# Performance work log

Measured on AMD Instinct MI355X. Metric: run time of the kernel, lower is better.

Reference implementation:

```python
import jax, jax.numpy as jnp
import numpy as np

N = 8192      # nodes
F = 256       # input feature dim
D_OUT = 256   # output_dim


def setup_inputs() -> dict:
    key = jax.random.key(0)
    k1, k2, k3 = jax.random.split(key, 3)
    data = jax.random.normal(k1, (1, N, F), dtype=jnp.float32)
    # dense (normalized) adjacency; the original converts dense->sparse then matmuls,
    # which is mathematically a dense adj @ data product.
    adj = jax.random.uniform(k2, (1, N, N), dtype=jnp.float32)
    kernel = jax.random.normal(k3, (F, D_OUT), dtype=jnp.float32)
    return {"data": data, "adj": adj, "kernel": kernel}


def reference(data, adj, kernel):
    # af = adj @ data  : [N, N] @ [N, F] -> [N, F]  (neighbor aggregation)
    af = jnp.matmul(adj[0], data[0])
    # dense projection: [N, F] @ [F, D_OUT] -> [N, D_OUT]
    out = jnp.matmul(af, kernel)
    # expand batch dim back and apply activation (relu)
    return jax.nn.relu(out[None, :, :])
```

## Files before the change

kernel.cpp:

```cpp
#include <hip/hip_runtime.h>
#include <stdint.h>

#define AS1 __attribute__((address_space(1)))
#define AS3 __attribute__((address_space(3)))

typedef float f32x4 __attribute__((ext_vector_type(4)));
typedef __bf16 bf16x8 __attribute__((ext_vector_type(8)));
typedef uint32_t u32x2 __attribute__((ext_vector_type(2)));
typedef unsigned short u16;
typedef u16 u16x8 __attribute__((ext_vector_type(8)));

__device__ __forceinline__ unsigned short f2bf(float f) {
    uint32_t x = __float_as_uint(f);
    x += 0x7FFFu + ((x >> 16) & 1u);
    return (unsigned short)(x >> 16);
}
__device__ __forceinline__ float bf2f(unsigned short u) {
    return __uint_as_float((uint32_t)u << 16);
}

__device__ __forceinline__ void gload_lds16(const void* g, void* l) {
    __builtin_amdgcn_global_load_lds((const AS1 void*)g, (AS3 void*)l, 16, 0, 0);
}

__global__ __launch_bounds__(256) void wt_kernel(const float* __restrict__ W,
                                                 unsigned short* __restrict__ WT) {
    __shared__ float tile[32][33];
    const int bf = blockIdx.x & 7;
    const int bn = blockIdx.x >> 3;
    const int t = threadIdx.x;
    const int c = t & 31, r = t >> 5;
#pragma unroll
    for (int i = 0; i < 4; ++i)
        tile[r + i * 8][c] = W[(bf * 32 + r + i * 8) * 256 + bn * 32 + c];
    __syncthreads();
#pragma unroll
    for (int i = 0; i < 4; ++i)
        WT[(bn * 32 + r + i * 8) * 256 + bf * 32 + c] = f2bf(tile[c][r + i * 8]);
}

template <int LDA, int LDB, int KSTEPS>
__global__ __launch_bounds__(256) void gemm1_kernel(const float* __restrict__ A,
                                                    const unsigned short* __restrict__ B,
                                                    unsigned short* __restrict__ dkT) {
    __shared__ unsigned short Alds[32 * 64];
    __shared__ unsigned short Blds[256 * 64];

    const int t = threadIdx.x;
    const int w = t >> 6;
    const int l = t & 63;
    const int m0 = blockIdx.x * 32;

    const int ar = t >> 3;
    const int kq = t & 7;
    const float* gA = A + (size_t)(m0 + ar) * LDA + kq * 4;
    char* aw0 = (char*)Alds + ((ar * 128 + kq * 8) ^ ((ar & 7) << 4));
    char* aw1 = (char*)Alds + ((ar * 128 + 64 + kq * 8) ^ ((ar & 7) << 4));

    const int nr_base = w * 64 + (l >> 3);
    const int c16 = l & 7;

    f32x4 acc[2][4];
#pragma unroll
    for (int i = 0; i < 2; ++i)
#pragma unroll
        for (int j = 0; j < 4; ++j) acc[i][j] = (f32x4){0.f, 0.f, 0.f, 0.f};

    for (int step = 0; step < KSTEPS; ++step) {
        const int k0 = step * 64;
        __syncthreads();
#pragma unroll
        for (int i = 0; i < 8; ++i) {
            const int nr = nr_base + i * 8;
            const unsigned short* src =
                B + (size_t)nr * LDB + k0 + ((c16 ^ (nr & 7)) << 3);
            gload_lds16(src, (char*)Blds + (w * 512 + i * 64) * 16);
        }
        const f32x4 v0 = *(const f32x4*)(gA + k0);
        const f32x4 v1 = *(const f32x4*)(gA + k0 + 32);
        uint32_t p0 = (uint32_t)f2bf(v0.x) | ((uint32_t)f2bf(v0.y) << 16);
        uint32_t p1 = (uint32_t)f2bf(v0.z) | ((uint32_t)f2bf(v0.w) << 16);
        uint32_t p2 = (uint32_t)f2bf(v1.x) | ((uint32_t)f2bf(v1.y) << 16);
        uint32_t p3 = (uint32_t)f2bf(v1.z) | ((uint32_t)f2bf(v1.w) << 16);
        ((uint32_t*)aw0)[0] = p0;
        ((uint32_t*)aw0)[1] = p1;
        ((uint32_t*)aw1)[0] = p2;
        ((uint32_t*)aw1)[1] = p3;
        __syncthreads();
#pragma unroll
        for (int kh = 0; kh < 2; ++kh) {
            const int koffb = kh * 64 + ((l >> 4) << 4);
            bf16x8 af[2], bv[4];
#pragma unroll
            for (int im = 0; im < 2; ++im) {
                const int r = im * 16 + (l & 15);
                af[im] = *(const bf16x8*)((const char*)Alds +
                                          ((r * 128 + koffb) ^ ((r & 7) << 4)));
            }
#pragma unroll
            for (int jn = 0; jn < 4; ++jn) {
                const int n = w * 64 + jn * 16 + (l & 15);
                bv[jn] = *(const bf16x8*)((const char*)Blds +
                                          ((n * 128 + koffb) ^ ((n & 7) << 4)));
            }
#pragma unroll
            for (int im = 0; im < 2; ++im)
#pragma unroll
                for (int jn = 0; jn < 4; ++jn)
                    acc[im][jn] = __builtin_amdgcn_mfma_f32_16x16x32_bf16(
                        af[im], bv[jn], acc[im][jn], 0, 0, 0);
        }
    }

    __syncthreads();
    u16* T = (u16*)Blds;
#pragma unroll
    for (int im = 0; im < 2; ++im) {
        const int mq = im * 16 + ((l >> 4) << 2);
#pragma unroll
        for (int jn = 0; jn < 4; ++jn) {
            const int n = w * 64 + jn * 16 + (l & 15);
            u32x2 pk;
            pk[0] = (uint32_t)f2bf(acc[im][jn][0]) |
                    ((uint32_t)f2bf(acc[im][jn][1]) << 16);
            pk[1] = (uint32_t)f2bf(acc[im][jn][2]) |
                    ((uint32_t)f2bf(acc[im][jn][3]) << 16);
            *(u32x2*)((char*)T + n * 80 + mq * 2) = pk;
        }
    }
    __syncthreads();
    {
        const int n = t;
        const char* src = (const char*)T + n * 80;
        char* dst = (char*)(dkT + (size_t)n * 8192 + m0);
#pragma unroll
        for (int i = 0; i < 4; ++i)
            *(f32x4*)(dst + i * 16) = *(const f32x4*)(src + i * 16);
    }
}

template <int KSPLIT>
__global__ __launch_bounds__(512) void gemm2_kernel(const float* __restrict__ A,
                                                    const unsigned short* __restrict__ B,
                                                    float* __restrict__ Out0,
                                                    u16* __restrict__ Pws) {
    __shared__ unsigned short Alds[128 * 64];
    __shared__ unsigned short Blds[256 * 64];

    const int t = threadIdx.x;
    const int w = t >> 6;
    const int l = t & 63;
    const int wr = w >> 2;
    const int wc = w & 3;
    const int q = l >> 4;
    const int li = l & 15;
    const int mtile = blockIdx.x / KSPLIT;
    const int ks = blockIdx.x % KSPLIT;
    const int m0 = mtile * 128;
    const int kbase = ks * (8192 / KSPLIT);
    constexpr int KSTEPS = (8192 / KSPLIT) / 64;

    const int rr0 = t >> 4;
    const int jc = t & 15;
    const float* gA = A + (size_t)(m0 + rr0) * 8192 + kbase + jc * 4;
    const int ap = (jc >> 1) ^ (rr0 & 7);
    char* const awbase = (char*)Alds + rr0 * 128 + ap * 16 + (jc & 1) * 8;

    const int br0 = t >> 3;
    const int c16 = t & 7;
    const unsigned short* gB =
        B + (size_t)br0 * 8192 + kbase + ((c16 ^ (br0 & 7)) << 3);

    f32x4 acc[4][4];
#pragma unroll
    for (int i = 0; i < 4; ++i)
#pragma unroll
        for (int j = 0; j < 4; ++j) acc[i][j] = (f32x4){0.f, 0.f, 0.f, 0.f};

    for (int step = 0; step < KSTEPS; ++step) {
        const int k0 = step * 64;
        __syncthreads();
#pragma unroll
        for (int i = 0; i < 4; ++i)
            gload_lds16(gB + (size_t)i * 64 * 8192 + k0,
                        (char*)Blds + (i * 512 + w * 64) * 16);
#pragma unroll
        for (int j = 0; j < 4; ++j) {
            const f32x4 v = *(const f32x4*)(gA + (size_t)j * 32 * 8192 + k0);
            u32x2 pk;
            pk[0] = (uint32_t)f2bf(v.x) | ((uint32_t)f2bf(v.y) << 16);
            pk[1] = (uint32_t)f2bf(v.z) | ((uint32_t)f2bf(v.w) << 16);
            *(u32x2*)(awbase + j * 32 * 128) = pk;
        }
        __syncthreads();
#pragma unroll
        for (int kh = 0; kh < 2; ++kh) {
            const int koffb = kh * 64 + (q << 4);
            bf16x8 af[4], bv[4];
#pragma unroll
            for (int im = 0; im < 4; ++im) {
                const int r = wr * 64 + im * 16 + li;
                af[im] = *(const bf16x8*)((const char*)Alds +
                                          ((r * 128 + koffb) ^ ((r & 7) << 4)));
            }
#pragma unroll
            for (int jn = 0; jn < 4; ++jn) {
                const int n = wc * 64 + jn * 16 + li;
                bv[jn] = *(const bf16x8*)((const char*)Blds +
                                          ((n * 128 + koffb) ^ ((n & 7) << 4)));
            }
#pragma unroll
            for (int im = 0; im < 4; ++im)
#pragma unroll
                for (int jn = 0; jn < 4; ++jn)
                    acc[im][jn] = __builtin_amdgcn_mfma_f32_16x16x32_bf16(
                        af[im], bv[jn], acc[im][jn], 0, 0, 0);
        }
    }

    if (KSPLIT == 1) {
#pragma unroll
        for (int im = 0; im < 4; ++im) {
            const int row0 = m0 + wr * 64 + im * 16 + (q << 2);
#pragma unroll
            for (int jn = 0; jn < 4; ++jn) {
                const int col = wc * 64 + jn * 16 + li;
#pragma unroll
                for (int r = 0; r < 4; ++r) {
                    const float v = acc[im][jn][r];
                    Out0[(size_t)(row0 + r) * 256 + col] = v > 0.f ? v : 0.f;
                }
            }
        }
    } else {
        u16* Pb = Pws + (size_t)ks * (8192 * 256);
#pragma unroll
        for (int im = 0; im < 4; ++im) {
            const int row0 = m0 + wr * 64 + im * 16 + (q << 2);
#pragma unroll
            for (int jn = 0; jn < 4; ++jn) {
                const int col = wc * 64 + jn * 16 + li;
#pragma unroll
                for (int r = 0; r < 4; ++r)
                    Pb[(size_t)(row0 + r) * 256 + col] = f2bf(acc[im][jn][r]);
            }
        }
    }
}

template <int S>
__global__ __launch_bounds__(256) void reduce_relu_kernel(float* __restrict__ out,
                                                          const u16* __restrict__ P) {
    const size_t i = (size_t)blockIdx.x * 256 + threadIdx.x;
    float s0 = 0, s1 = 0, s2 = 0, s3 = 0, s4 = 0, s5 = 0, s6 = 0, s7 = 0;
#pragma unroll
    for (int s = 0; s < S; ++s) {
        const u16x8 v = ((const u16x8*)(P + (size_t)s * (8192 * 256)))[i];
        s0 += bf2f(v[0]); s1 += bf2f(v[1]); s2 += bf2f(v[2]); s3 += bf2f(v[3]);
        s4 += bf2f(v[4]); s5 += bf2f(v[5]); s6 += bf2f(v[6]); s7 += bf2f(v[7]);
    }
    f32x4 lo, hi;
    lo.x = s0 > 0.f ? s0 : 0.f; lo.y = s1 > 0.f ? s1 : 0.f;
    lo.z = s2 > 0.f ? s2 : 0.f; lo.w = s3 > 0.f ? s3 : 0.f;
    hi.x = s4 > 0.f ? s4 : 0.f; hi.y = s5 > 0.f ? s5 : 0.f;
    hi.z = s6 > 0.f ? s6 : 0.f; hi.w = s7 > 0.f ? s7 : 0.f;
    ((f32x4*)out)[2 * i] = lo;
    ((f32x4*)out)[2 * i + 1] = hi;
}

extern "C" void kernel_launch(void* const* d_in, const int* in_sizes, int n_in,
                              void* d_out, int out_size, void* d_ws, size_t ws_size,
                              hipStream_t stream) {
    const float* data = (const float*)d_in[0];
    const float* adj = (const float*)d_in[1];
    const float* Wk = (const float*)d_in[2];
    float* out = (float*)d_out;

    unsigned short* WT = (unsigned short*)d_ws;
    unsigned short* dkT = (unsigned short*)((char*)d_ws + 131072);
    u16* Pb = (u16*)((char*)d_ws + 131072 + 4194304);

    const size_t base_need = 131072 + 4194304;
    const size_t part_bytes = (size_t)8192 * 256 * 2;

    wt_kernel<<<64, 256, 0, stream>>>(Wk, WT);
    gemm1_kernel<256, 256, 4><<<256, 256, 0, stream>>>(data, WT, dkT);
    if (ws_size >= base_need + 8 * part_bytes) {
        gemm2_kernel<8><<<512, 512, 0, stream>>>(adj, dkT, out, Pb);
        reduce_relu_kernel<8><<<1024, 256, 0, stream>>>(out, Pb);
    } else if (ws_size >= base_need + 2 * part_bytes) {
        gemm2_kernel<2><<<128, 512, 0, stream>>>(adj, dkT, out, Pb);
        reduce_relu_kernel<2><<<1024, 256, 0, stream>>>(out, Pb);
    } else {
        gemm2_kernel<1><<<64, 512, 0, stream>>>(adj, dkT, out, nullptr);
    }
}
```

Measured before the change: 98.45 us.

## Double-buffer B tile in LDS and prefetch A into registers

Software-pipelines the gemm2 main loop. The next K-step's B tile is loaded into a second LDS buffer and the next A fp32 values are loaded into registers while the current step's MFMAs run. One of the two per-step barriers is replaced by an explicit lgkmcnt wait plus s_barrier. This is meant to hide global-load latency behind compute, at the cost of twice the B LDS footprint (lower occupancy) and extra registers. The barrier waits only on lgkmcnt and not vmcnt, so correctness depends on the compiler inserting the wait for the async LDS loads.

```diff
diff --git a/kernel.cpp b/kernel.cpp
--- a/kernel.cpp
+++ b/kernel.cpp
@@ -145,7 +145,7 @@
                                                     float* __restrict__ Out0,
                                                     u16* __restrict__ Pws) {
     __shared__ unsigned short Alds[128 * 64];
-    __shared__ unsigned short Blds[256 * 64];
+    __shared__ unsigned short Bls[2][256 * 64];
 
     const int t = threadIdx.x;
     const int w = t >> 6;
@@ -177,22 +177,40 @@
 #pragma unroll
         for (int j = 0; j < 4; ++j) acc[i][j] = (f32x4){0.f, 0.f, 0.f, 0.f};
 
-    for (int step = 0; step < KSTEPS; ++step) {
-        const int k0 = step * 64;
+    f32x4 ra[4];
+#pragma unroll
+    for (int i = 0; i < 4; ++i)
+        gload_lds16(gB + (size_t)i * 64 * 8192,
+                    (char*)Bls[0] + (i * 512 + w * 64) * 16);
+#pragma unroll
+    for (int j = 0; j < 4; ++j)
+        ra[j] = *(const f32x4*)(gA + (size_t)j * 32 * 8192);
+
+    for (int st = 0; st < KSTEPS; ++st) {
         __syncthreads();
-#pragma unroll
-        for (int i = 0; i < 4; ++i)
-            gload_lds16(gB + (size_t)i * 64 * 8192 + k0,
-                        (char*)Blds + (i * 512 + w * 64) * 16);
+        const int k1 = (st + 1) * 64;
+        if (st + 1 < KSTEPS) {
+#pragma unroll
+            for (int i = 0; i < 4; ++i)
+                gload_lds16(gB + (size_t)i * 64 * 8192 + k1,
+                            (char*)Bls[(st + 1) & 1] + (i * 512 + w * 64) * 16);
+        }
 #pragma unroll
         for (int j = 0; j < 4; ++j) {
-            const f32x4 v = *(const f32x4*)(gA + (size_t)j * 32 * 8192 + k0);
             u32x2 pk;
-            pk[0] = (uint32_t)f2bf(v.x) | ((uint32_t)f2bf(v.y) << 16);
-            pk[1] = (uint32_t)f2bf(v.z) | ((uint32_t)f2bf(v.w) << 16);
+            pk[0] = (uint32_t)f2bf(ra[j].x) | ((uint32_t)f2bf(ra[j].y) << 16);
+            pk[1] = (uint32_t)f2bf(ra[j].z) | ((uint32_t)f2bf(ra[j].w) << 16);
             *(u32x2*)(awbase + j * 32 * 128) = pk;
         }
-        __syncthreads();
+        if (st + 1 < KSTEPS) {
+#pragma unroll
+            for (int j = 0; j < 4; ++j)
+                ra[j] = *(const f32x4*)(gA + (size_t)j * 32 * 8192 + k1);
+        }
+        asm volatile("s_waitcnt lgkmcnt(0)" ::: "memory");
+        __builtin_amdgcn_s_barrier();
+        __builtin_amdgcn_sched_barrier(0);
+        const char* Bcur = (const char*)Bls[st & 1];
 #pragma unroll
         for (int kh = 0; kh < 2; ++kh) {
             const int koffb = kh * 64 + (q << 4);
@@ -206,7 +224,7 @@
 #pragma unroll
             for (int jn = 0; jn < 4; ++jn) {
                 const int n = wc * 64 + jn * 16 + li;
-                bv[jn] = *(const bf16x8*)((const char*)Blds +
+                bv[jn] = *(const bf16x8*)(Bcur +
                                           ((n * 128 + koffb) ^ ((n & 7) << 4)));
             }
 #pragma unroll
```

New measurement: 107.3 us. 9.0% more time.
